# Performance work log

Measured on AMD Instinct MI355X. Metric: run time of the kernel, lower is better.

Reference implementation:

```python
import jax, jax.numpy as jnp
import numpy as np

N = 20000       # nodes
E = 500000      # edges
D = 256         # dim_in == dim_out (residual requires equality)
T = 4           # num_layers
NTYPES = 3      # cfg.edge_types = [0, 1, 2]
NU = 1          # cfg nu; nu_v2 = False -> delay = max(k - NU, 0) = k - 1


def setup_inputs() -> dict:
    key = jax.random.key(0)
    ks = jax.random.split(key, 8)
    x = jax.random.normal(ks[0], (N, D), dtype=jnp.float32)
    edge_index = jax.random.randint(ks[1], (2, E), 0, N, dtype=jnp.int32)
    hop = jax.random.randint(ks[2], (E,), 1, T + 1, dtype=jnp.int32)   # k in 1..T
    etype = jax.random.randint(ks[3], (E,), 0, NTYPES, dtype=jnp.int32)
    edge_attr = jnp.stack([hop, etype], axis=1)  # [E, 2]
    scale = 0.05
    W_edge = scale * jax.random.normal(ks[4], (T, NTYPES, D, D), dtype=jnp.float32)
    b_edge = scale * jax.random.normal(ks[5], (T, NTYPES, D), dtype=jnp.float32)
    # hop layers W(k, t) for k in 2..t+1; index (t, k-2); max k = T -> T-1 slots
    W_hop = scale * jax.random.normal(ks[6], (T, T - 1, D, D), dtype=jnp.float32)
    b_hop = scale * jax.random.normal(ks[7], (T, T - 1, D), dtype=jnp.float32)
    return {"x": x, "edge_index": edge_index, "edge_attr": edge_attr,
            "W_edge": W_edge, "b_edge": b_edge, "W_hop": W_hop, "b_hop": b_hop}


def _gnn_layer(h_src, src, dst, mask, n_nodes):
    # GNNLayer: linear transform at source nodes then sum-aggregate over the
    # masked edge subset (equivalent to restricting edge_index to that subset).
    msg = jnp.where(mask[:, None], h_src[src], jnp.float32(0.0))  # [E, D]
    return jax.ops.segment_sum(msg, dst, num_segments=n_nodes)    # [N, D]


def reference(x, edge_index, edge_attr, W_edge, b_edge, W_hop, b_hop):
    n_nodes = x.shape[0]
    src, dst = edge_index[0], edge_index[1]
    hop, etype = edge_attr[:, 0], edge_attr[:, 1]
    xs = []
    for t in range(T):
        xs.append(x)
        acc = jnp.zeros_like(x)
        # 1-hop relational layers, one per edge type e
        for e in range(NTYPES):
            h = xs[t] @ W_edge[t, e] + b_edge[t, e]          # transform at node level
            acc = acc + _gnn_layer(h, src, dst, etype == e, n_nodes)
        # delayed multi-hop layers, k = 2..t+1, reading x[t - delay]
        for k in range(2, t + 2):
            delay = max(k - NU, 0)  # nu_v2 = False
            h = xs[t - delay] @ W_hop[t, k - 2] + b_hop[t, k - 2]
            acc = acc + _gnn_layer(h, src, dst, hop == k, n_nodes)
        x = xs[t] + jax.nn.relu(acc)  # residual; cfg.gnn.l2norm = False
    return x
```

## Files before the change

kernel.cpp:

```cpp
#include <hip/hip_runtime.h>


#define NN 20000
#define NROWP 20032
#define NE 500000
#define DD 256
#define TT 4
#define NT 3
#define NB 118

typedef _Float16 f16;
typedef _Float16 f16x8 __attribute__((ext_vector_type(8)));
typedef _Float16 f16x4v __attribute__((ext_vector_type(4)));
typedef float f32x4 __attribute__((ext_vector_type(4)));
typedef int i32x4a __attribute__((ext_vector_type(4), aligned(4)));

__device__ inline void f4add(float4& a, const float4 b) {
  a.x += b.x; a.y += b.y; a.z += b.z; a.w += b.w;
}

__device__ __forceinline__ void gload_lds16(const void* g, void* l) {
  __builtin_amdgcn_global_load_lds(
      (const __attribute__((address_space(1))) unsigned int*)g,
      (__attribute__((address_space(3))) unsigned int*)l, 16, 0, 0);
}


__global__ void k_hist(const int* __restrict__ ei, const int* __restrict__ ea,
                       int* __restrict__ cnt) {
  int e = blockIdx.x * 256 + threadIdx.x;
  if (e >= NE) return;
  int dst = ei[NE + e];
  int hop = ea[2 * e];
  int et  = ea[2 * e + 1];
  atomicAdd(&cnt[et * NN + dst], 1);
  if (hop >= 2) atomicAdd(&cnt[(3 + hop - 2) * NN + dst], 1);
}


__global__ __launch_bounds__(1024) void k_scan_blk(
    const int* __restrict__ cnt, int* __restrict__ crow, int* __restrict__ bsum) {
  __shared__ int wsum[16];
  int tid = threadIdx.x, lane = tid & 63, wv = tid >> 6;
  int i = blockIdx.x * 1024 + tid;
  int v = (i < 6 * NN) ? cnt[i] : 0;
  int s = v;
#pragma unroll
  for (int off = 1; off < 64; off <<= 1) {
    int t = __shfl_up(s, off, 64);
    if (lane >= off) s += t;
  }
  if (lane == 63) wsum[wv] = s;
  __syncthreads();
  if (wv == 0) {
    int ws = (lane < 16) ? wsum[lane] : 0;
#pragma unroll
    for (int off = 1; off < 16; off <<= 1) {
      int t = __shfl_up(ws, off, 64);
      if (lane >= off) ws += t;
    }
    if (lane < 16) wsum[lane] = ws;
  }
  __syncthreads();
  int excl = ((wv == 0) ? 0 : wsum[wv - 1]) + s - v;
  if (i < 6 * NN) crow[i] = excl;
  if (tid == 1023) bsum[blockIdx.x] = wsum[15];
}

__global__ __launch_bounds__(128) void k_scan_top(
    int* __restrict__ bsum, int* __restrict__ crow) {
  __shared__ int wsum2[2];
  int tid = threadIdx.x, lane = tid & 63, wv = tid >> 6;
  int v = (tid < NB) ? bsum[tid] : 0;
  int s = v;
#pragma unroll
  for (int off = 1; off < 64; off <<= 1) {
    int t = __shfl_up(s, off, 64);
    if (lane >= off) s += t;
  }
  if (lane == 63) wsum2[wv] = s;
  __syncthreads();
  int add = (wv == 1) ? wsum2[0] : 0;
  int excl = add + s - v;
  if (tid < NB) bsum[tid] = excl;
  if (tid == NB - 1) crow[6 * NN] = excl + v;
}

__global__ __launch_bounds__(1024) void k_scan_fix(
    int* __restrict__ crow, int* __restrict__ ccur, const int* __restrict__ bsum) {
  int i = blockIdx.x * 1024 + threadIdx.x;
  if (i >= 6 * NN) return;
  int val = crow[i] + bsum[blockIdx.x];
  crow[i] = val;
  ccur[i] = val;
}

__global__ void k_scatter(const int* __restrict__ ei, const int* __restrict__ ea,
                          int* __restrict__ ccur, int* __restrict__ crec) {
  int e = blockIdx.x * 256 + threadIdx.x;
  if (e >= NE) return;
  int src = ei[e];
  int dst = ei[NE + e];
  int hop = ea[2 * e];
  int et  = ea[2 * e + 1];
  int pos = atomicAdd(&ccur[et * NN + dst], 1);
  crec[pos] = src;
  if (hop >= 2) {
    int pos2 = atomicAdd(&ccur[(3 + hop - 2) * NN + dst], 1);
    crec[pos2] = src;
  }
}


__global__ __launch_bounds__(256) void k_wsplit(
    const float* __restrict__ W_edge, const float* __restrict__ W_hop,
    f16* __restrict__ Wout) {
  __shared__ float tile[64][65];
  int w = blockIdx.z;
  int tk = blockIdx.x * 64;
  int tn = blockIdx.y * 64;
  const float* src = (w < 12) ? (W_edge + (size_t)w * 65536)
                              : (W_hop + (size_t)(w - 12) * 65536);
  f16* dst = Wout + (size_t)w * 65536;
  int c = threadIdx.x & 63;
  int r0 = threadIdx.x >> 6;
#pragma unroll
  for (int i = 0; i < 16; i++) {
    int r = i * 4 + r0;
    tile[r][c] = src[(size_t)(tk + r) * 256 + tn + c] * 16.0f;
  }
  __syncthreads();
#pragma unroll
  for (int i = 0; i < 16; i++) {
    int r = i * 4 + r0;
    dst[(size_t)(tn + r) * 256 + tk + c] = (f16)tile[c][r];
  }
}


__global__ void k_xcast(const float* __restrict__ x, f16* __restrict__ xh) {
  size_t i = (size_t)(blockIdx.x * 256 + threadIdx.x) * 4;
  float4 v = *(const float4*)(x + i);
  f16x4v h = { (f16)v.x, (f16)v.y, (f16)v.z, (f16)v.w };
  *(f16x4v*)(xh + i) = h;
}


struct AggArgs {
  f16* out[6];
};

__global__ __launch_bounds__(256) void k_aggregate(
    const f16* __restrict__ xh,
    const int* __restrict__ crow,
    const int* __restrict__ crec,
    AggArgs args)
{
  int ch = blockIdx.y;
  f16* outp = args.out[ch];
  if (!outp) return;
  int wave = threadIdx.x >> 6;
  int lane = threadIdx.x & 63;
  int half = lane >> 5;
  int chunk = lane & 31;
  int v = blockIdx.x * 4 + wave;
  int base = ch * NN + v;
  int beg = crow[base], end = crow[base + 1];
  const char* xb = (const char*)xh + chunk * 16;
  float acc[8];
#pragma unroll
  for (int j = 0; j < 8; j++) acc[j] = 0.f;

  int e = beg;
  for (; e + 8 <= end; e += 8) {
    i32x4a i0 = *(const i32x4a*)(crec + e);
    i32x4a i1 = *(const i32x4a*)(crec + e + 4);
    int s0 = half ? i0.y : i0.x;
    int s1 = half ? i0.w : i0.z;
    int s2 = half ? i1.y : i1.x;
    int s3 = half ? i1.w : i1.z;
    f16x8 h0 = *(const f16x8*)(xb + (size_t)s0 * 512);
    f16x8 h1 = *(const f16x8*)(xb + (size_t)s1 * 512);
    f16x8 h2 = *(const f16x8*)(xb + (size_t)s2 * 512);
    f16x8 h3 = *(const f16x8*)(xb + (size_t)s3 * 512);
#pragma unroll
    for (int j = 0; j < 8; j++) {
      float a = (float)h0[j] + (float)h1[j];
      float b = (float)h2[j] + (float)h3[j];
      acc[j] += a + b;
    }
  }
  for (; e + 2 <= end; e += 2) {
    int s0 = crec[e + half];
    f16x8 h0 = *(const f16x8*)(xb + (size_t)s0 * 512);
#pragma unroll
    for (int j = 0; j < 8; j++) acc[j] += (float)h0[j];
  }
  if (e < end) {
    if (half == 0) {
      int s0 = crec[e];
      f16x8 h0 = *(const f16x8*)(xb + (size_t)s0 * 512);
#pragma unroll
      for (int j = 0; j < 8; j++) acc[j] += (float)h0[j];
    }
  }
#pragma unroll
  for (int j = 0; j < 8; j++) acc[j] += __shfl_xor(acc[j], 32, 64);
  if (half == 0) {
    const float s = 0.015625f;
    f16x8 o;
#pragma unroll
    for (int j = 0; j < 8; j++) o[j] = (f16)(acc[j] * s);
    *(f16x8*)((char*)outp + (size_t)v * 512 + chunk * 16) = o;
  }
}


struct GemmArgs {
  const f16* A[6];
  const f16* W[6];
  const float* bias[6];
  const int*   cnt[6];
  int nch;
  int write_f32;
  const f16* xh_in;
  f16*       xh_out;
  float*     f32_out;
};

__global__ __launch_bounds__(256) void k_gemm(GemmArgs args) {
  __shared__ __align__(16) f16 sA[2][4096];
  __shared__ __align__(16) f16 sB[2][8192];
  const int tid = threadIdx.x;
  const int lane = tid & 63;
  const int wave = tid >> 6;
  const int wm = (wave >> 1) * 32;
  const int wn = (wave & 1) * 64;
  const int m0 = blockIdx.x * 64;
  const int n0 = blockIdx.y * 128;
  const int nch = args.nch;
  const int Titer = nch * 4;

  f32x4 acc[2][4];
#pragma unroll
  for (int mi = 0; mi < 2; mi++)
#pragma unroll
    for (int ni = 0; ni < 4; ni++) acc[mi][ni] = (f32x4){0.f, 0.f, 0.f, 0.f};

  int srcA[2], ldsAoff[2];
#pragma unroll
  for (int i = 0; i < 2; i++) {
    int g = wave + i * 4;
    int s = g * 64 + lane;
    int ks = s >> 8, r = (s >> 2) & 63, pc = s & 3;
    int lc = pc ^ ((r >> 1) & 3);
    srcA[i] = r * 512 + ks * 64 + lc * 16;
    ldsAoff[i] = g * 1024;
  }
  int srcB[4], ldsBoff[4];
#pragma unroll
  for (int i = 0; i < 4; i++) {
    int g = wave + i * 4;
    int s = g * 64 + lane;
    int ks = s >> 9, r = (s >> 2) & 127, pc = s & 3;
    int lc = pc ^ ((r >> 1) & 3);
    srcB[i] = r * 512 + ks * 64 + lc * 16;
    ldsBoff[i] = g * 1024;
  }

  const int fr = lane & 15;
  const int gq = lane >> 4;
  int offA[2][2], offB[4][2];
#pragma unroll
  for (int mi = 0; mi < 2; mi++) {
    int rr = wm + mi * 16 + fr;
    int swz = (gq ^ ((rr >> 1) & 3)) << 4;
#pragma unroll
    for (int ks = 0; ks < 2; ks++) offA[mi][ks] = ks * 4096 + rr * 64 + swz;
  }
#pragma unroll
  for (int ni = 0; ni < 4; ni++) {
    int rr = wn + ni * 16 + fr;
    int swz = (gq ^ ((rr >> 1) & 3)) << 4;
#pragma unroll
    for (int ks = 0; ks < 2; ks++) offB[ni][ks] = ks * 8192 + rr * 64 + swz;
  }

  auto stage = [&](int buf, int j) {
    int c = j >> 2, kb = (j & 3) * 128;
    const char* pa = (const char*)args.A[c] + (size_t)m0 * 512 + kb;
    const char* pb = (const char*)args.W[c] + (size_t)n0 * 512 + kb;
#pragma unroll
    for (int i = 0; i < 2; i++)
      gload_lds16(pa + srcA[i], (char*)sA[buf] + ldsAoff[i]);
#pragma unroll
    for (int i = 0; i < 4; i++)
      gload_lds16(pb + srcB[i], (char*)sB[buf] + ldsBoff[i]);
  };

  stage(0, 0);
  stage(1, 1);

  for (int j = 0; j < Titer; ++j) {
    const int p = j & 1;
    if (j + 1 < Titer) {
      asm volatile("s_waitcnt vmcnt(6)" ::: "memory");
    } else {
      asm volatile("s_waitcnt vmcnt(0)" ::: "memory");
    }
    __builtin_amdgcn_s_barrier();
    __builtin_amdgcn_sched_barrier(0);
    {
      f16x8 fA[2][2], fB[2][4];
#pragma unroll
      for (int ks = 0; ks < 2; ks++) {
#pragma unroll
        for (int mi = 0; mi < 2; mi++)
          fA[ks][mi] = *(const f16x8*)((const char*)sA[p] + offA[mi][ks]);
#pragma unroll
        for (int ni = 0; ni < 4; ni++)
          fB[ks][ni] = *(const f16x8*)((const char*)sB[p] + offB[ni][ks]);
      }
#pragma unroll
      for (int ks = 0; ks < 2; ks++)
#pragma unroll
        for (int mi = 0; mi < 2; mi++)
#pragma unroll
          for (int ni = 0; ni < 4; ni++)
            acc[mi][ni] = __builtin_amdgcn_mfma_f32_16x16x32_f16(
                fA[ks][mi], fB[ks][ni], acc[mi][ni], 0, 0, 0);
    }
    __builtin_amdgcn_s_barrier();
    __builtin_amdgcn_sched_barrier(0);
    if (j + 2 < Titer) stage(p, j + 2);
  }

  float bcol[4][6];
#pragma unroll
  for (int ni = 0; ni < 4; ni++) {
    int gcol = n0 + wn + ni * 16 + fr;
#pragma unroll
    for (int c = 0; c < 6; c++)
      bcol[ni][c] = (c < nch) ? args.bias[c][gcol] : 0.f;
  }
  const int rowq = gq * 4;
#pragma unroll
  for (int mi = 0; mi < 2; mi++) {
#pragma unroll
    for (int rI = 0; rI < 4; rI++) {
      int grow = m0 + wm + mi * 16 + rowq + rI;
      if (grow < NN) {
        float cv[6];
#pragma unroll
        for (int c = 0; c < 6; c++)
          cv[c] = (c < nch) ? (float)args.cnt[c][grow] : 0.f;
        size_t rowoff = (size_t)grow * DD;
#pragma unroll
        for (int ni = 0; ni < 4; ni++) {
          int gcol = n0 + wn + ni * 16 + fr;
          float v = acc[mi][ni][rI] * 4.0f;
#pragma unroll
          for (int c = 0; c < 6; c++) v += cv[c] * bcol[ni][c];
          float outv = (float)args.xh_in[rowoff + gcol] + fmaxf(v, 0.f);
          args.xh_out[rowoff + gcol] = (f16)outv;
          if (args.write_f32) args.f32_out[rowoff + gcol] = outv;
        }
      }
    }
  }
}


extern "C" void kernel_launch(void* const* d_in, const int* in_sizes, int n_in,
                              void* d_out, int out_size, void* d_ws, size_t ws_size,
                              hipStream_t stream) {
  const float* x      = (const float*)d_in[0];
  const int* edge_index = (const int*)d_in[1];
  const int* edge_attr  = (const int*)d_in[2];
  const float* W_edge = (const float*)d_in[3];
  const float* b_edge = (const float*)d_in[4];
  const float* W_hop  = (const float*)d_in[5];
  const float* b_hop  = (const float*)d_in[6];
  float* out = (float*)d_out;

  char* ws = (char*)d_ws;
  int* cnt  = (int*)ws;
  int* crow = cnt + 6 * NN;
  int* ccur = crow + 6 * NN + 1;
  int* bsum = ccur + 6 * NN;
  int* crec = bsum + NB;
  size_t int_count = (size_t)6 * NN + (6 * NN + 1) + 6 * NN + NB + 2 * (size_t)NE;
  const size_t ND  = (size_t)NN * DD;
  const size_t NDP = (size_t)NROWP * DD;
  f16* Wsplit = (f16*)(ws + ((int_count * 4 + 255) & ~(size_t)255));
  f16* xh = Wsplit + (size_t)24 * 65536;
  f16* aggBase = xh + ND;
  f16* agg[9];
  for (int i = 0; i < 9; i++) agg[i] = aggBase + (size_t)i * NDP;
  f16** Cb = agg + 3;

  hipMemsetAsync(cnt, 0, 6 * NN * sizeof(int), stream);

  k_hist<<<(NE + 255) / 256, 256, 0, stream>>>(edge_index, edge_attr, cnt);
  k_scan_blk<<<NB, 1024, 0, stream>>>(cnt, crow, bsum);
  k_scan_top<<<1, 128, 0, stream>>>(bsum, crow);
  k_scan_fix<<<NB, 1024, 0, stream>>>(crow, ccur, bsum);
  k_scatter<<<(NE + 255) / 256, 256, 0, stream>>>(edge_index, edge_attr, ccur, crec);
  k_wsplit<<<dim3(4, 4, 24), 256, 0, stream>>>(W_edge, W_hop, Wsplit);
  k_xcast<<<ND / 1024, 256, 0, stream>>>(x, xh);

  for (int t = 0; t < TT; ++t) {
    AggArgs aa{};
    aa.out[0] = agg[0];
    aa.out[1] = agg[1];
    aa.out[2] = agg[2];
    aa.out[3] = (t <= 2) ? Cb[t]     : nullptr;
    aa.out[4] = (t <= 1) ? Cb[3 + t] : nullptr;
    aa.out[5] = (t == 0) ? Cb[5]     : nullptr;
    k_aggregate<<<dim3(NN / 4, 6), 256, 0, stream>>>(xh, crow, crec, aa);

    GemmArgs ga{};
    for (int e = 0; e < NT; ++e) {
      ga.A[e]    = agg[e];
      ga.W[e]    = Wsplit + (size_t)(t * NT + e) * 65536;
      ga.bias[e] = b_edge + (size_t)(t * NT + e) * DD;
      ga.cnt[e]  = cnt + (size_t)e * NN;
    }
    int nc = NT;
    for (int k = 2; k <= t + 1; ++k) {
      int s = t + 1 - k;
      ga.A[nc]    = (k == 2) ? Cb[s] : (k == 3) ? Cb[3 + s] : Cb[5];
      ga.W[nc]    = Wsplit + (size_t)(12 + t * 3 + (k - 2)) * 65536;
      ga.bias[nc] = b_hop + (size_t)(t * (TT - 1) + (k - 2)) * DD;
      ga.cnt[nc]  = cnt + (size_t)(3 + (k - 2)) * NN;
      nc++;
    }
    for (int c = nc; c < 6; ++c) {
      ga.A[c] = ga.A[0]; ga.W[c] = ga.W[0]; ga.bias[c] = ga.bias[0]; ga.cnt[c] = ga.cnt[0];
    }
    ga.nch = nc;
    ga.write_f32 = (t == TT - 1) ? 1 : 0;
    ga.xh_in  = xh;
    ga.xh_out = xh;
    ga.f32_out = out;
    k_gemm<<<dim3(313, 2), 256, 0, stream>>>(ga);
  }
}
```

Baseline: 536.4 us.

## Bucket edges by node, type and hop so one gather feeds all aggregates

Replaces the six separate CSR channels (three edge types plus three hop groups, with hop edges stored twice) with a single CSR keyed by (dst, etype, hop). The aggregation kernel now walks each node's edges once, adding every gathered row to both its edge-type accumulator and, when needed, its hop accumulator. A small kernel rebuilds the per-channel counts the GEMM still uses. This aims to roughly halve gather traffic and edge-index storage, at the cost of a larger scan, more registers and less parallelism per block.

```diff
diff --git a/kernel.cpp b/kernel.cpp
--- a/kernel.cpp
+++ b/kernel.cpp
@@ -7,17 +7,13 @@
 #define DD 256
 #define TT 4
 #define NT 3
-#define NB 118
+#define SCANN (12 * NN)
+#define NB12 235
 
 typedef _Float16 f16;
 typedef _Float16 f16x8 __attribute__((ext_vector_type(8)));
 typedef _Float16 f16x4v __attribute__((ext_vector_type(4)));
 typedef float f32x4 __attribute__((ext_vector_type(4)));
-typedef int i32x4a __attribute__((ext_vector_type(4), aligned(4)));
-
-__device__ inline void f4add(float4& a, const float4 b) {
-  a.x += b.x; a.y += b.y; a.z += b.z; a.w += b.w;
-}
 
 __device__ __forceinline__ void gload_lds16(const void* g, void* l) {
   __builtin_amdgcn_global_load_lds(
@@ -27,14 +23,13 @@
 
 
 __global__ void k_hist(const int* __restrict__ ei, const int* __restrict__ ea,
-                       int* __restrict__ cnt) {
+                       int* __restrict__ cnt12) {
   int e = blockIdx.x * 256 + threadIdx.x;
   if (e >= NE) return;
   int dst = ei[NE + e];
   int hop = ea[2 * e];
   int et  = ea[2 * e + 1];
-  atomicAdd(&cnt[et * NN + dst], 1);
-  if (hop >= 2) atomicAdd(&cnt[(3 + hop - 2) * NN + dst], 1);
+  atomicAdd(&cnt12[((dst * 3 + et) << 2) | (hop - 1)], 1);
 }
 
 
@@ -43,7 +38,7 @@
   __shared__ int wsum[16];
   int tid = threadIdx.x, lane = tid & 63, wv = tid >> 6;
   int i = blockIdx.x * 1024 + tid;
-  int v = (i < 6 * NN) ? cnt[i] : 0;
+  int v = (i < SCANN) ? cnt[i] : 0;
   int s = v;
 #pragma unroll
   for (int off = 1; off < 64; off <<= 1) {
@@ -63,15 +58,15 @@
   }
   __syncthreads();
   int excl = ((wv == 0) ? 0 : wsum[wv - 1]) + s - v;
-  if (i < 6 * NN) crow[i] = excl;
+  if (i < SCANN) crow[i] = excl;
   if (tid == 1023) bsum[blockIdx.x] = wsum[15];
 }
 
-__global__ __launch_bounds__(128) void k_scan_top(
+__global__ __launch_bounds__(256) void k_scan_top(
     int* __restrict__ bsum, int* __restrict__ crow) {
-  __shared__ int wsum2[2];
+  __shared__ int wsum2[4];
   int tid = threadIdx.x, lane = tid & 63, wv = tid >> 6;
-  int v = (tid < NB) ? bsum[tid] : 0;
+  int v = (tid < NB12) ? bsum[tid] : 0;
   int s = v;
 #pragma unroll
   for (int off = 1; off < 64; off <<= 1) {
@@ -80,16 +75,18 @@
   }
   if (lane == 63) wsum2[wv] = s;
   __syncthreads();
-  int add = (wv == 1) ? wsum2[0] : 0;
+  int add = 0;
+#pragma unroll
+  for (int w = 0; w < 4; w++) add += (w < wv) ? wsum2[w] : 0;
   int excl = add + s - v;
-  if (tid < NB) bsum[tid] = excl;
-  if (tid == NB - 1) crow[6 * NN] = excl + v;
+  if (tid < NB12) bsum[tid] = excl;
+  if (tid == NB12 - 1) crow[SCANN] = excl + v;
 }
 
 __global__ __launch_bounds__(1024) void k_scan_fix(
     int* __restrict__ crow, int* __restrict__ ccur, const int* __restrict__ bsum) {
   int i = blockIdx.x * 1024 + threadIdx.x;
-  if (i >= 6 * NN) return;
+  if (i >= SCANN) return;
   int val = crow[i] + bsum[blockIdx.x];
   crow[i] = val;
   ccur[i] = val;
@@ -103,12 +100,29 @@
   int dst = ei[NE + e];
   int hop = ea[2 * e];
   int et  = ea[2 * e + 1];
-  int pos = atomicAdd(&ccur[et * NN + dst], 1);
+  int pos = atomicAdd(&ccur[((dst * 3 + et) << 2) | (hop - 1)], 1);
   crec[pos] = src;
-  if (hop >= 2) {
-    int pos2 = atomicAdd(&ccur[(3 + hop - 2) * NN + dst], 1);
-    crec[pos2] = src;
-  }
+}
+
+
+__global__ __launch_bounds__(256) void k_cnt6(
+    const int* __restrict__ crow12, int* __restrict__ cnt) {
+  int v = blockIdx.x * 256 + threadIdx.x;
+  if (v >= NN) return;
+  int h2 = 0, h3 = 0, h4 = 0;
+#pragma unroll
+  for (int et = 0; et < 3; et++) {
+    int base = (v * 3 + et) * 4;
+    int b0 = crow12[base], b1 = crow12[base + 1], b2 = crow12[base + 2],
+        b3 = crow12[base + 3], b4 = crow12[base + 4];
+    cnt[et * NN + v] = b4 - b0;
+    h2 += b2 - b1;
+    h3 += b3 - b2;
+    h4 += b4 - b3;
+  }
+  cnt[3 * NN + v] = h2;
+  cnt[4 * NN + v] = h3;
+  cnt[5 * NN + v] = h4;
 }
 
 
@@ -150,68 +164,121 @@
   f16* out[6];
 };
 
+#define GSEG(LO, HI, DOH, ACCH)                                         \
+  {                                                                     \
+    int e_ = (LO);                                                      \
+    for (; e_ + 4 <= (HI); e_ += 4) {                                   \
+      int s0_ = crec[e_ + half], s1_ = crec[e_ + 2 + half];             \
+      f16x8 h0_ = *(const f16x8*)(xb + (size_t)s0_ * 512);              \
+      f16x8 h1_ = *(const f16x8*)(xb + (size_t)s1_ * 512);              \
+      float tb_[8];                                                     \
+      _Pragma("unroll") for (int j = 0; j < 8; j++) {                   \
+        tb_[j] = (float)h0_[j] + (float)h1_[j];                         \
+        aE[j] += tb_[j];                                                \
+      }                                                                 \
+      if (DOH) {                                                        \
+        _Pragma("unroll") for (int j = 0; j < 8; j++) ACCH[j] += tb_[j];\
+      }                                                                 \
+    }                                                                   \
+    if (e_ + 2 <= (HI)) {                                               \
+      int s0_ = crec[e_ + half];                                        \
+      f16x8 h0_ = *(const f16x8*)(xb + (size_t)s0_ * 512);              \
+      float tb_[8];                                                     \
+      _Pragma("unroll") for (int j = 0; j < 8; j++) {                   \
+        tb_[j] = (float)h0_[j];                                         \
+        aE[j] += tb_[j];                                                \
+      }                                                                 \
+      if (DOH) {                                                        \
+        _Pragma("unroll") for (int j = 0; j < 8; j++) ACCH[j] += tb_[j];\
+      }                                                                 \
+      e_ += 2;                                                          \
+    }                                                                   \
+    if (e_ < (HI) && half == 0) {                                       \
+      int s0_ = crec[e_];                                               \
+      f16x8 h0_ = *(const f16x8*)(xb + (size_t)s0_ * 512);              \
+      float tb_[8];                                                     \
+      _Pragma("unroll") for (int j = 0; j < 8; j++) {                   \
+        tb_[j] = (float)h0_[j];                                         \
+        aE[j] += tb_[j];                                                \
+      }                                                                 \
+      if (DOH) {                                                        \
+        _Pragma("unroll") for (int j = 0; j < 8; j++) ACCH[j] += tb_[j];\
+      }                                                                 \
+    }                                                                   \
+  }
+
 __global__ __launch_bounds__(256) void k_aggregate(
     const f16* __restrict__ xh,
-    const int* __restrict__ crow,
+    const int* __restrict__ crow12,
     const int* __restrict__ crec,
     AggArgs args)
 {
-  int ch = blockIdx.y;
-  f16* outp = args.out[ch];
-  if (!outp) return;
   int wave = threadIdx.x >> 6;
   int lane = threadIdx.x & 63;
   int half = lane >> 5;
   int chunk = lane & 31;
   int v = blockIdx.x * 4 + wave;
-  int base = ch * NN + v;
-  int beg = crow[base], end = crow[base + 1];
   const char* xb = (const char*)xh + chunk * 16;
-  float acc[8];
-#pragma unroll
-  for (int j = 0; j < 8; j++) acc[j] = 0.f;
-
-  int e = beg;
-  for (; e + 8 <= end; e += 8) {
-    i32x4a i0 = *(const i32x4a*)(crec + e);
-    i32x4a i1 = *(const i32x4a*)(crec + e + 4);
-    int s0 = half ? i0.y : i0.x;
-    int s1 = half ? i0.w : i0.z;
-    int s2 = half ? i1.y : i1.x;
-    int s3 = half ? i1.w : i1.z;
-    f16x8 h0 = *(const f16x8*)(xb + (size_t)s0 * 512);
-    f16x8 h1 = *(const f16x8*)(xb + (size_t)s1 * 512);
-    f16x8 h2 = *(const f16x8*)(xb + (size_t)s2 * 512);
-    f16x8 h3 = *(const f16x8*)(xb + (size_t)s3 * 512);
-#pragma unroll
-    for (int j = 0; j < 8; j++) {
-      float a = (float)h0[j] + (float)h1[j];
-      float b = (float)h2[j] + (float)h3[j];
-      acc[j] += a + b;
-    }
-  }
-  for (; e + 2 <= end; e += 2) {
-    int s0 = crec[e + half];
-    f16x8 h0 = *(const f16x8*)(xb + (size_t)s0 * 512);
-#pragma unroll
-    for (int j = 0; j < 8; j++) acc[j] += (float)h0[j];
-  }
-  if (e < end) {
+  const bool doH2 = (args.out[3] != nullptr);
+  const bool doH3 = (args.out[4] != nullptr);
+  const bool doH4 = (args.out[5] != nullptr);
+  const float s = 0.015625f;
+
+  float aH2[8], aH3[8], aH4[8];
+#pragma unroll
+  for (int j = 0; j < 8; j++) { aH2[j] = 0.f; aH3[j] = 0.f; aH4[j] = 0.f; }
+
+#pragma unroll
+  for (int et = 0; et < 3; et++) {
+    int base = (v * 3 + et) * 4;
+    int b0 = crow12[base], b1 = crow12[base + 1], b2 = crow12[base + 2],
+        b3 = crow12[base + 3], b4 = crow12[base + 4];
+    float aE[8];
+#pragma unroll
+    for (int j = 0; j < 8; j++) aE[j] = 0.f;
+    GSEG(b0, b1, false, aH2);
+    GSEG(b1, b2, doH2, aH2);
+    GSEG(b2, b3, doH3, aH3);
+    GSEG(b3, b4, doH4, aH4);
+#pragma unroll
+    for (int j = 0; j < 8; j++) aE[j] += __shfl_xor(aE[j], 32, 64);
     if (half == 0) {
-      int s0 = crec[e];
-      f16x8 h0 = *(const f16x8*)(xb + (size_t)s0 * 512);
-#pragma unroll
-      for (int j = 0; j < 8; j++) acc[j] += (float)h0[j];
-    }
-  }
-#pragma unroll
-  for (int j = 0; j < 8; j++) acc[j] += __shfl_xor(acc[j], 32, 64);
-  if (half == 0) {
-    const float s = 0.015625f;
-    f16x8 o;
-#pragma unroll
-    for (int j = 0; j < 8; j++) o[j] = (f16)(acc[j] * s);
-    *(f16x8*)((char*)outp + (size_t)v * 512 + chunk * 16) = o;
+      f16x8 o;
+#pragma unroll
+      for (int j = 0; j < 8; j++) o[j] = (f16)(aE[j] * s);
+      *(f16x8*)((char*)args.out[et] + (size_t)v * 512 + chunk * 16) = o;
+    }
+  }
+
+  if (doH2) {
+#pragma unroll
+    for (int j = 0; j < 8; j++) aH2[j] += __shfl_xor(aH2[j], 32, 64);
+    if (half == 0) {
+      f16x8 o;
+#pragma unroll
+      for (int j = 0; j < 8; j++) o[j] = (f16)(aH2[j] * s);
+      *(f16x8*)((char*)args.out[3] + (size_t)v * 512 + chunk * 16) = o;
+    }
+  }
+  if (doH3) {
+#pragma unroll
+    for (int j = 0; j < 8; j++) aH3[j] += __shfl_xor(aH3[j], 32, 64);
+    if (half == 0) {
+      f16x8 o;
+#pragma unroll
+      for (int j = 0; j < 8; j++) o[j] = (f16)(aH3[j] * s);
+      *(f16x8*)((char*)args.out[4] + (size_t)v * 512 + chunk * 16) = o;
+    }
+  }
+  if (doH4) {
+#pragma unroll
+    for (int j = 0; j < 8; j++) aH4[j] += __shfl_xor(aH4[j], 32, 64);
+    if (half == 0) {
+      f16x8 o;
+#pragma unroll
+      for (int j = 0; j < 8; j++) o[j] = (f16)(aH4[j] * s);
+      *(f16x8*)((char*)args.out[5] + (size_t)v * 512 + chunk * 16) = o;
+    }
   }
 }
 
@@ -384,12 +451,12 @@
   float* out = (float*)d_out;
 
   char* ws = (char*)d_ws;
-  int* cnt  = (int*)ws;
-  int* crow = cnt + 6 * NN;
-  int* ccur = crow + 6 * NN + 1;
-  int* bsum = ccur + 6 * NN;
-  int* crec = bsum + NB;
-  size_t int_count = (size_t)6 * NN + (6 * NN + 1) + 6 * NN + NB + 2 * (size_t)NE;
+  int* cnt    = (int*)ws;
+  int* crow12 = cnt + 6 * NN;
+  int* ccur12 = crow12 + SCANN + 1;
+  int* bsum   = ccur12 + SCANN;
+  int* crec   = bsum + NB12;
+  size_t int_count = (size_t)6 * NN + (SCANN + 1) + SCANN + NB12 + (size_t)NE;
   const size_t ND  = (size_t)NN * DD;
   const size_t NDP = (size_t)NROWP * DD;
   f16* Wsplit = (f16*)(ws + ((int_count * 4 + 255) & ~(size_t)255));
@@ -399,13 +466,14 @@
   for (int i = 0; i < 9; i++) agg[i] = aggBase + (size_t)i * NDP;
   f16** Cb = agg + 3;
 
-  hipMemsetAsync(cnt, 0, 6 * NN * sizeof(int), stream);
-
-  k_hist<<<(NE + 255) / 256, 256, 0, stream>>>(edge_index, edge_attr, cnt);
-  k_scan_blk<<<NB, 1024, 0, stream>>>(cnt, crow, bsum);
-  k_scan_top<<<1, 128, 0, stream>>>(bsum, crow);
-  k_scan_fix<<<NB, 1024, 0, stream>>>(crow, ccur, bsum);
-  k_scatter<<<(NE + 255) / 256, 256, 0, stream>>>(edge_index, edge_attr, ccur, crec);
+  hipMemsetAsync(ccur12, 0, SCANN * sizeof(int), stream);
+
+  k_hist<<<(NE + 255) / 256, 256, 0, stream>>>(edge_index, edge_attr, ccur12);
+  k_scan_blk<<<NB12, 1024, 0, stream>>>(ccur12, crow12, bsum);
+  k_scan_top<<<1, 256, 0, stream>>>(bsum, crow12);
+  k_scan_fix<<<NB12, 1024, 0, stream>>>(crow12, ccur12, bsum);
+  k_scatter<<<(NE + 255) / 256, 256, 0, stream>>>(edge_index, edge_attr, ccur12, crec);
+  k_cnt6<<<(NN + 255) / 256, 256, 0, stream>>>(crow12, cnt);
   k_wsplit<<<dim3(4, 4, 24), 256, 0, stream>>>(W_edge, W_hop, Wsplit);
   k_xcast<<<ND / 1024, 256, 0, stream>>>(x, xh);
 
@@ -417,7 +485,7 @@
     aa.out[3] = (t <= 2) ? Cb[t]     : nullptr;
     aa.out[4] = (t <= 1) ? Cb[3 + t] : nullptr;
     aa.out[5] = (t == 0) ? Cb[5]     : nullptr;
-    k_aggregate<<<dim3(NN / 4, 6), 256, 0, stream>>>(xh, crow, crec, aa);
+    k_aggregate<<<dim3(NN / 4), 256, 0, stream>>>(xh, crow12, crec, aa);
 
     GemmArgs ga{};
     for (int e = 0; e < NT; ++e) {
```

Result: faster. 490.8 us (-8.5%).
